# Optimization experiments

Hardware: AMD Instinct MI355X
Metric: run time of the kernel (lower is better)

## Reference

```python
import jax, jax.numpy as jnp
import numpy as np
from jax import lax

# Fixed dims from MSSMamba defaults
B_, L_, DM = 2, 8192, 256
NH, HP, NS = 4, 64, 8          # nheads, headdim, d_state
DIN = NH * HP                  # d_inner = 256
DPROJ = 2 * DIN + 2 * NS + NH  # 532


def setup_inputs() -> dict:
    key = jax.random.key(0)
    ks = jax.random.split(key, 16)
    f = lambda k, s, sc=1.0: jax.random.normal(k, s, jnp.float32) * sc
    inp = {
        'x_H': f(ks[0], (B_, L_, DM)),
        'x_V': f(ks[1], (B_, L_, DM)),
        'W_in_H': f(ks[2], (DM, 2 * DPROJ), 0.05),
        'W_in_V': f(ks[3], (DM, 2 * DPROJ), 0.05),
        'W_out_HF': f(ks[4], (DIN, DM), 0.05),
        'W_out_HB': f(ks[5], (DIN, DM), 0.05),
        'W_out_VF': f(ks[6], (DIN, DM), 0.05),
        'W_out_VB': f(ks[7], (DIN, DM), 0.05),
        'W_out': f(ks[8], (4 * DM, DM), 0.05),
    }
    for i, nm in enumerate(['HF', 'HB', 'VF', 'VB']):
        kd = jax.random.fold_in(ks[9], i)
        ka = jax.random.fold_in(ks[10], i)
        inp['dt_bias_' + nm] = f(kd, (NH,), 0.1)
        inp['A_log_' + nm] = jnp.log(jax.random.uniform(ka, (NH,), jnp.float32, 1.0, 16.0))
        inp['D_' + nm] = jnp.ones((NH,), jnp.float32)
    # per-batch permutation mapping vertical position -> horizontal position
    inp['v2h'] = jax.vmap(lambda k: jax.random.permutation(k, L_))(
        jax.random.split(ks[11], B_)).astype(jnp.int32)
    return inp


def _scan_dir(zxbcdt, dt_bias, A_log, D):
    # zxbcdt: [b, l, DPROJ] -> Mamba2-style selective scan, ngroups=1
    z = zxbcdt[..., :DIN].reshape(B_, L_, NH, HP)
    xBC = jax.nn.silu(zxbcdt[..., DIN:DIN + DIN + 2 * NS])
    x = xBC[..., :DIN].reshape(B_, L_, NH, HP)
    Bm = xBC[..., DIN:DIN + NS]      # [b, l, n]
    Cm = xBC[..., DIN + NS:]         # [b, l, n]
    dt = jax.nn.softplus(zxbcdt[..., -NH:] + dt_bias)  # [b, l, h]
    A = -jnp.exp(A_log)              # [h]
    dA = jnp.exp(dt * A)             # [b, l, h]
    dBx = jnp.einsum('blh,bln,blhp->blhpn', dt, Bm, x)  # [b,l,h,p,n]

    def step(state, inp):
        dA_t, dBx_t, C_t = inp
        state = dA_t[..., None, None] * state + dBx_t   # [b,h,p,n]
        y_t = jnp.einsum('bhpn,bn->bhp', state, C_t)
        return state, y_t

    init = jnp.zeros((B_, NH, HP, NS), dt.dtype)
    _, ys = lax.scan(step, init, (jnp.moveaxis(dA, 1, 0),
                                  jnp.moveaxis(dBx, 1, 0),
                                  jnp.moveaxis(Cm, 1, 0)))
    y = jnp.moveaxis(ys, 0, 1) + D[None, None, :, None] * x  # skip D*x
    y = y * jax.nn.silu(z)                                   # gate
    return y.reshape(B_, L_, DIN)


def reference(x_H, x_V, W_in_H, W_in_V,
              dt_bias_HF, dt_bias_HB, dt_bias_VF, dt_bias_VB,
              A_log_HF, A_log_HB, A_log_VF, A_log_VB,
              D_HF, D_HB, D_VF, D_VB,
              W_out_HF, W_out_HB, W_out_VF, W_out_VB,
              W_out, v2h):
    zx_HF, zx_HB = jnp.split(x_H @ W_in_H, 2, axis=-1)
    zx_VF, zx_VB = jnp.split(x_V @ W_in_V, 2, axis=-1)
    # note: source applies out_proj_HB to the HF branch (kept faithful)
    y_HF = _scan_dir(zx_HF, dt_bias_HF, A_log_HF, D_HF) @ W_out_HB
    y_HB = _scan_dir(zx_HB[:, ::-1], dt_bias_HB, A_log_HB, D_HB)[:, ::-1] @ W_out_HF
    y_VF = _scan_dir(zx_VF, dt_bias_VF, A_log_VF, D_VF) @ W_out_VB
    y_VB = _scan_dir(zx_VB[:, ::-1], dt_bias_VB, A_log_VB, D_VB)[:, ::-1] @ W_out_VF
    # remap vertical-ordered outputs to horizontal ordering (scatter by v2h)
    bidx = jnp.arange(B_)[:, None]
    y_VF = jnp.zeros_like(y_VF).at[bidx, v2h].set(y_VF)
    y_VB = jnp.zeros_like(y_VB).at[bidx, v2h].set(y_VB)
    cat = jnp.concatenate([y_HF, y_HB, y_VF, y_VB], axis=-1)  # [b, l, 4*d_model]
    return jax.nn.silu(cat) @ W_out
```

## Files before the change

### kernel.cpp

```cpp
#include <hip/hip_runtime.h>
#include <hip/hip_bf16.h>

#define B_N 2
#define L_N 8192
#define ROWS 16384
#define CHUNK 32
#define NCHUNK 256
#define NPAD 1152

typedef __bf16 bf16x8 __attribute__((ext_vector_type(8)));
typedef float f32x4 __attribute__((ext_vector_type(4)));

__device__ __forceinline__ float siluf(float v) {
  return v * __builtin_amdgcn_rcpf(1.f + __expf(-v));
}
__device__ __forceinline__ float softplusf_(float v) {
  return fmaxf(v, 0.f) + log1pf(__expf(-fabsf(v)));
}
__device__ __forceinline__ unsigned short f2bf(float v) {
  union { __bf16 b; unsigned short u; } x;
  x.b = (__bf16)v;
  return x.u;
}
__device__ __forceinline__ float bf2f(unsigned short u) {
  union { unsigned u; float f; } x; x.u = ((unsigned)u) << 16;
  return x.f;
}

__device__ __forceinline__ void gload_lds16(const unsigned short* g, unsigned short* l) {
  __builtin_amdgcn_global_load_lds(
      (const __attribute__((address_space(1))) unsigned int*)g,
      (__attribute__((address_space(3))) unsigned int*)l, 16, 0, 0);
}

struct P4 { const float* p[4]; };

__global__ void k_prep_all(const float* __restrict__ xH, const float* __restrict__ xV,
                           const float* __restrict__ WH, const float* __restrict__ WV,
                           P4 ws, const float* __restrict__ W_out, const int* __restrict__ v2h,
                           unsigned short* __restrict__ xbf, unsigned short* __restrict__ Wt_in,
                           unsigned short* __restrict__ Wt_dirs, unsigned short* __restrict__ Wt_fin,
                           int* __restrict__ inv) {
  int bid = blockIdx.x;
  int tid = threadIdx.x;
  if (bid < 8192) {
    int mat = bid >> 12;
    int i = (bid & 4095) * 256 + tid;
    const float* s = mat ? xV : xH;
    float4 v = ((const float4*)s)[i];
    ushort4 o;
    o.x = f2bf(v.x); o.y = f2bf(v.y); o.z = f2bf(v.z); o.w = f2bf(v.w);
    ((ushort4*)(xbf + (size_t)mat * ROWS * 256))[i] = o;
  } else if (bid < 10496) {
    int i = (bid - 8192) * 256 + tid;
    int z = i / (NPAD * 256);
    int rem = i - z * (NPAD * 256);
    int n = rem >> 8, k = rem & 255;
    const float* W = z ? WV : WH;
    int sl = n >= 544;
    int cc = n - (sl ? 544 : 0);
    float v = (cc < 532) ? W[(long)k * 1064 + sl * 532 + cc] : 0.f;
    Wt_in[i] = f2bf(v);
  } else if (bid < 11520) {
    int i = (bid - 10496) * 256 + tid;
    int d = i >> 16;
    int rem = i & 65535;
    int n = rem >> 8, k = rem & 255;
    Wt_dirs[i] = f2bf(ws.p[d][(long)k * 256 + n]);
  } else if (bid < 12544) {
    int i = (bid - 11520) * 256 + tid;
    int n = i >> 10, k = i & 1023;
    Wt_fin[i] = f2bf(W_out[(long)k * 256 + n]);
  } else {
    int m = (bid - 12544) * 256 + tid;
    if (m < ROWS) {
      int b = m >> 13;
      inv[b * L_N + v2h[m]] = m;
    }
  }
}

struct ScanConsts {
  const float* dt_bias[4];
  const float* A_log[4];
  const float* D[4];
};

__global__ __launch_bounds__(256) void k_dtfix(
    const float* __restrict__ xH, const float* __restrict__ xV,
    const float* __restrict__ WH, const float* __restrict__ WV,
    ScanConsts sc, float* __restrict__ dtv_arr, float* __restrict__ dA_arr) {
  __shared__ float xs[32][257];
  __shared__ float Wsm[8][260];
  const int mat = blockIdx.y;
  const float* x = mat ? xV : xH;
  const float* W = mat ? WV : WH;
  const int r0 = blockIdx.x * 32;
  for (int i = threadIdx.x; i < 2048; i += 256) {
    int c = i >> 8, k = i & 255;
    int sl = c >> 2, h = c & 3;
    Wsm[c][k] = W[(long)k * 1064 + sl * 532 + 528 + h];
  }
  for (int i = threadIdx.x; i < 32 * 64; i += 256) {
    int rl = i >> 6, kq = (i & 63) * 4;
    float4 v = *(const float4*)(x + (long)(r0 + rl) * 256 + kq);
    xs[rl][kq + 0] = v.x; xs[rl][kq + 1] = v.y; xs[rl][kq + 2] = v.z; xs[rl][kq + 3] = v.w;
  }
  __syncthreads();
  const int rl = threadIdx.x >> 3, c = threadIdx.x & 7;
  float s = 0.f;
  #pragma unroll 8
  for (int k = 0; k < 256; ++k) s = fmaf(xs[rl][k], Wsm[c][k], s);
  const int sl = c >> 2, h = c & 3;
  const int dir = mat * 2 + sl;
  float dtv = softplusf_(s + sc.dt_bias[dir][h]);
  float dAv = __expf(dtv * (-__expf(sc.A_log[dir][h])));
  long o = ((long)dir * 4 + h) * ROWS + (r0 + rl);
  dtv_arr[o] = dtv;
  dA_arr[o] = dAv;
}

struct EpiIn {
  unsigned short* zsil;
  unsigned short* xsil;
  unsigned short* bc;
};

__global__ __launch_bounds__(256) void k_gemm_in(
    const unsigned short* __restrict__ Abase, const unsigned short* __restrict__ Btbase,
    EpiIn ep) {
  __shared__ unsigned short As[128 * 32];
  __shared__ unsigned short Bs[128 * 32];
  __shared__ unsigned short trs[4][16 * 72];
  const int tid = threadIdx.x;
  const int lane = tid & 63;
  const int wid = tid >> 6;
  const int wm = wid & 1, wn = wid >> 1;
  const int q = lane >> 4, r = lane & 15;
  const int m0 = blockIdx.x * 128;
  const int n0 = blockIdx.y * 128;
  const int z = blockIdx.z;
  const unsigned short* A = Abase + (long)z * ROWS * 256;
  const unsigned short* Bt = Btbase + (long)z * NPAD * 256;

  f32x4 acc[4][4] = {};
  const int swr = (r >> 1) & 3;

  for (int kt = 0; kt < 256; kt += 32) {
    #pragma unroll
    for (int i = 0; i < 2; ++i) {
      int idx = i * 256 + tid;
      int row = idx >> 2;
      int ch = (idx & 3) ^ ((row >> 1) & 3);
      gload_lds16(A + (long)(m0 + row) * 256 + kt + ch * 8,
                  &As[(size_t)(i * 256 + wid * 64) * 8]);
    }
    #pragma unroll
    for (int i = 0; i < 2; ++i) {
      int idx = i * 256 + tid;
      int row = idx >> 2;
      int ch = (idx & 3) ^ ((row >> 1) & 3);
      gload_lds16(Bt + (long)(n0 + row) * 256 + kt + ch * 8,
                  &Bs[(size_t)(i * 256 + wid * 64) * 8]);
    }
    __syncthreads();
    bf16x8 af[4], bfr[4];
    #pragma unroll
    for (int mi = 0; mi < 4; ++mi)
      af[mi] = *(const bf16x8*)&As[((wm * 64 + mi * 16 + r) * 4 + (q ^ swr)) * 8];
    #pragma unroll
    for (int ni = 0; ni < 4; ++ni)
      bfr[ni] = *(const bf16x8*)&Bs[((wn * 64 + ni * 16 + r) * 4 + (q ^ swr)) * 8];
    #pragma unroll
    for (int mi = 0; mi < 4; ++mi)
      #pragma unroll
      for (int ni = 0; ni < 4; ++ni)
        acc[mi][ni] = __builtin_amdgcn_mfma_f32_16x16x32_bf16(af[mi], bfr[ni], acc[mi][ni], 0, 0, 0);
    __syncthreads();
  }

  unsigned short* tr = trs[wid];
  #pragma unroll
  for (int mi = 0; mi < 4; ++mi) {
    #pragma unroll
    for (int ni = 0; ni < 4; ++ni)
      #pragma unroll
      for (int j = 0; j < 4; ++j)
        tr[(q * 4 + j) * 72 + ni * 16 + r] = f2bf(siluf(acc[mi][ni][j]));
    asm volatile("s_waitcnt lgkmcnt(0)" ::: "memory");
    #pragma unroll
    for (int pass = 0; pass < 2; ++pass) {
      int rl = pass * 8 + (lane >> 3);
      int c8 = (lane & 7) * 8;
      bf16x8 v = *(const bf16x8*)&tr[rl * 72 + c8];
      int row = m0 + wm * 64 + mi * 16 + rl;
      int col = n0 + wn * 64 + c8;
      int sl = col >= 544;
      int cc = col - (sl ? 544 : 0);
      if (cc < 528) {
        int dir = z * 2 + sl;
        if (cc < 256)
          *(bf16x8*)(ep.zsil + ((long)dir * ROWS + row) * 256 + cc) = v;
        else if (cc < 512)
          *(bf16x8*)(ep.xsil + ((long)dir * ROWS + row) * 256 + cc - 256) = v;
        else
          *(bf16x8*)(ep.bc + ((long)dir * ROWS + row) * 16 + cc - 512) = v;
      }
    }
    asm volatile("s_waitcnt lgkmcnt(0)" ::: "memory");
  }
}

__global__ __launch_bounds__(256) void k_fuse(
    const unsigned short* __restrict__ ybf,
    const unsigned short* __restrict__ Wt_dirs,
    const unsigned short* __restrict__ Wt_fin,
    const int* __restrict__ inv,
    unsigned short* __restrict__ pbuf) {
  __shared__ unsigned short Tl[64][264];
  __shared__ unsigned short As1[64 * 32];
  __shared__ unsigned short Bs1[256 * 32];
  __shared__ int arow[64];
  const int tid = threadIdx.x;
  const int lane = tid & 63;
  const int wid = tid >> 6;
  const int q = lane >> 4, r = lane & 15;
  const int r0 = blockIdx.x * 64;
  const int pair = blockIdx.y;
  const int swr = (r >> 1) & 3;

  if (tid < 64) arow[tid] = pair ? inv[r0 + tid] : (r0 + tid);
  __syncthreads();

  f32x4 acc_o[4][4] = {};

  #pragma unroll
  for (int dd = 0; dd < 2; ++dd) {
    const int d = pair * 2 + dd;
    const unsigned short* yd = ybf + (long)d * ROWS * 256;
    const unsigned short* Wd = Wt_dirs + (long)d * 65536;

    f32x4 acc_t[4][4] = {};
    for (int kt = 0; kt < 256; kt += 32) {
      {
        int row = tid >> 2;
        int ch = (tid & 3) ^ ((row >> 1) & 3);
        gload_lds16(yd + (long)arow[row] * 256 + kt + ch * 8, &As1[(size_t)(wid * 64) * 8]);
      }
      #pragma unroll
      for (int i = 0; i < 4; ++i) {
        int idx = i * 256 + tid;
        int row = idx >> 2;
        int ch = (idx & 3) ^ ((row >> 1) & 3);
        gload_lds16(Wd + (long)row * 256 + kt + ch * 8,
                    &Bs1[(size_t)(i * 256 + wid * 64) * 8]);
      }
      __syncthreads();
      bf16x8 af[4], bfr[4];
      #pragma unroll
      for (int mi = 0; mi < 4; ++mi)
        af[mi] = *(const bf16x8*)&As1[((mi * 16 + r) * 4 + (q ^ swr)) * 8];
      #pragma unroll
      for (int ni = 0; ni < 4; ++ni)
        bfr[ni] = *(const bf16x8*)&Bs1[((wid * 64 + ni * 16 + r) * 4 + (q ^ swr)) * 8];
      #pragma unroll
      for (int mi = 0; mi < 4; ++mi)
        #pragma unroll
        for (int ni = 0; ni < 4; ++ni)
          acc_t[mi][ni] = __builtin_amdgcn_mfma_f32_16x16x32_bf16(af[mi], bfr[ni], acc_t[mi][ni], 0, 0, 0);
      __syncthreads();
    }
    #pragma unroll
    for (int mi = 0; mi < 4; ++mi)
      #pragma unroll
      for (int ni = 0; ni < 4; ++ni)
        #pragma unroll
        for (int j = 0; j < 4; ++j)
          Tl[mi * 16 + q * 4 + j][wid * 64 + ni * 16 + r] = f2bf(siluf(acc_t[mi][ni][j]));
    __syncthreads();
    for (int kt = 0; kt < 256; kt += 32) {
      #pragma unroll
      for (int i = 0; i < 4; ++i) {
        int idx = i * 256 + tid;
        int row = idx >> 2;
        int ch = (idx & 3) ^ ((row >> 1) & 3);
        gload_lds16(Wt_fin + (long)row * 1024 + d * 256 + kt + ch * 8,
                    &Bs1[(size_t)(i * 256 + wid * 64) * 8]);
      }
      __syncthreads();
      bf16x8 af[4], bfr[4];
      #pragma unroll
      for (int mi = 0; mi < 4; ++mi)
        af[mi] = *(const bf16x8*)&Tl[mi * 16 + r][kt + q * 8];
      #pragma unroll
      for (int ni = 0; ni < 4; ++ni)
        bfr[ni] = *(const bf16x8*)&Bs1[((wid * 64 + ni * 16 + r) * 4 + (q ^ swr)) * 8];
      #pragma unroll
      for (int mi = 0; mi < 4; ++mi)
        #pragma unroll
        for (int ni = 0; ni < 4; ++ni)
          acc_o[mi][ni] = __builtin_amdgcn_mfma_f32_16x16x32_bf16(af[mi], bfr[ni], acc_o[mi][ni], 0, 0, 0);
      __syncthreads();
    }
  }

  #pragma unroll
  for (int mi = 0; mi < 4; ++mi)
    #pragma unroll
    for (int ni = 0; ni < 4; ++ni)
      #pragma unroll
      for (int j = 0; j < 4; ++j)
        Tl[mi * 16 + q * 4 + j][wid * 64 + ni * 16 + r] = f2bf(acc_o[mi][ni][j]);
  asm volatile("s_waitcnt lgkmcnt(0)" ::: "memory");
  unsigned short* pout = pbuf + (long)pair * ROWS * 256;
  #pragma unroll
  for (int pass = 0; pass < 8; ++pass) {
    int rl = pass * 8 + (lane >> 3);
    int c8 = (lane & 7) * 8;
    bf16x8 v = *(const bf16x8*)&Tl[rl][wid * 64 + c8];
    *(bf16x8*)(pout + (long)(r0 + rl) * 256 + wid * 64 + c8) = v;
  }
}

__global__ void k_red(const unsigned short* __restrict__ pbuf, float* __restrict__ out) {
  int i = blockIdx.x * 256 + threadIdx.x;
  uint4 a = ((const uint4*)pbuf)[i];
  uint4 b = ((const uint4*)(pbuf + (size_t)ROWS * 256))[i];
  const unsigned short* au = (const unsigned short*)&a;
  const unsigned short* bu = (const unsigned short*)&b;
  float rr[8];
  #pragma unroll
  for (int j = 0; j < 8; ++j) rr[j] = bf2f(au[j]) + bf2f(bu[j]);
  ((float4*)out)[i * 2] = *(float4*)&rr[0];
  ((float4*)out)[i * 2 + 1] = *(float4*)&rr[4];
}

struct ScanP {
  const unsigned short* xsil;
  const unsigned short* zsil;
  const unsigned short* bc;
  const float* dtv;
  const float* dA;
  const float* D[4];
};

__global__ __launch_bounds__(64) void k_scan1(ScanP sp, float* __restrict__ S,
                                              float* __restrict__ P) {
  __shared__ __align__(16) float Bst[CHUNK][8];
  __shared__ float dAs[CHUNK];
  const int p = threadIdx.x;
  const int c = blockIdx.x;
  const int bh = blockIdx.y;
  const int d = blockIdx.z;
  const int b = bh >> 2, h = bh & 3;
  const int rev = d & 1;
  const int t0 = c * CHUNK;
  if (p < CHUNK) {
    const int t = t0 + p;
    const int l = rev ? (L_N - 1 - t) : t;
    const int row = (b << 13) + l;
    uint4 bv = *(const uint4*)(sp.bc + ((long)d * ROWS + row) * 16);
    const unsigned short* bu = (const unsigned short*)&bv;
    float dtvv = sp.dtv[((long)d * 4 + h) * ROWS + row];
    dAs[p] = sp.dA[((long)d * 4 + h) * ROWS + row];
    #pragma unroll
    for (int n = 0; n < 8; ++n) Bst[p][n] = bf2f(bu[n]) * dtvv;
  }
  __syncthreads();

  float st[8] = {0, 0, 0, 0, 0, 0, 0, 0};
  float cumdA = 1.f;
  const int l0 = rev ? (L_N - 1 - t0) : t0;
  const unsigned short* xp = sp.xsil + ((long)d * ROWS + (b << 13) + l0) * 256 + h * 64 + p;
  const long stp = rev ? -256L : 256L;

  unsigned short xa[8], xb[8];
  #pragma unroll
  for (int j = 0; j < 8; ++j) xa[j] = xp[(long)j * stp];
  #pragma unroll
  for (int g = 0; g < 4; ++g) {
    if (g < 3) {
      #pragma unroll
      for (int j = 0; j < 8; ++j) xb[j] = xp[(long)((g + 1) * 8 + j) * stp];
    }
    #pragma unroll
    for (int j = 0; j < 8; ++j) {
      int s = g * 8 + j;
      float x = bf2f(xa[j]);
      float dA = dAs[s];
      f32x4 B0 = *(const f32x4*)&Bst[s][0];
      f32x4 B1 = *(const f32x4*)&Bst[s][4];
      cumdA *= dA;
      st[0] = fmaf(dA, st[0], x * B0[0]);
      st[1] = fmaf(dA, st[1], x * B0[1]);
      st[2] = fmaf(dA, st[2], x * B0[2]);
      st[3] = fmaf(dA, st[3], x * B0[3]);
      st[4] = fmaf(dA, st[4], x * B1[0]);
      st[5] = fmaf(dA, st[5], x * B1[1]);
      st[6] = fmaf(dA, st[6], x * B1[2]);
      st[7] = fmaf(dA, st[7], x * B1[3]);
    }
    #pragma unroll
    for (int j = 0; j < 8; ++j) xa[j] = xb[j];
  }
  float* Sp = S + ((((long)d * NCHUNK + c) * 8 + bh) * 64 + p) * 8;
  #pragma unroll
  for (int n = 0; n < 8; ++n) Sp[n] = st[n];
  if (p == 0) P[((long)d * NCHUNK + c) * 8 + bh] = cumdA;
}

__global__ __launch_bounds__(512) void k_scan2(const float* __restrict__ S,
                                               const float* __restrict__ P,
                                               float* __restrict__ carry) {
  __shared__ float Pl[NCHUNK];
  const int tid = threadIdx.x;
  const int dbh = blockIdx.x;
  const int d = dbh >> 3, bh = dbh & 7;
  if (tid < NCHUNK) Pl[tid] = P[((long)d * NCHUNK + tid) * 8 + bh];
  __syncthreads();
  float cy = 0.f;
  carry[(((long)d * NCHUNK + 0) * 8 + bh) * 512 + tid] = 0.f;
  #pragma unroll 8
  for (int c = 1; c < NCHUNK; ++c) {
    const float Sv = S[(((long)d * NCHUNK + (c - 1)) * 8 + bh) * 512 + tid];
    cy = fmaf(Pl[c - 1], cy, Sv);
    carry[(((long)d * NCHUNK + c) * 8 + bh) * 512 + tid] = cy;
  }
}

__global__ __launch_bounds__(64) void k_scan3(ScanP sp, const float* __restrict__ carry,
                                              unsigned short* __restrict__ ybf) {
  __shared__ __align__(16) float Bst[CHUNK][8];
  __shared__ __align__(16) float Cst[CHUNK][8];
  __shared__ float dAs[CHUNK];
  const int p = threadIdx.x;
  const int c = blockIdx.x;
  const int bh = blockIdx.y;
  const int d = blockIdx.z;
  const int b = bh >> 2, h = bh & 3;
  const int rev = d & 1;
  const float Dv = sp.D[d][h];
  const int t0 = c * CHUNK;
  if (p < CHUNK) {
    const int t = t0 + p;
    const int l = rev ? (L_N - 1 - t) : t;
    const int row = (b << 13) + l;
    const unsigned short* bp = sp.bc + ((long)d * ROWS + row) * 16;
    uint4 bv = *(const uint4*)bp;
    uint4 cv = *(const uint4*)(bp + 8);
    const unsigned short* bu = (const unsigned short*)&bv;
    const unsigned short* cu = (const unsigned short*)&cv;
    float dtvv = sp.dtv[((long)d * 4 + h) * ROWS + row];
    dAs[p] = sp.dA[((long)d * 4 + h) * ROWS + row];
    #pragma unroll
    for (int n = 0; n < 8; ++n) Bst[p][n] = bf2f(bu[n]) * dtvv;
    #pragma unroll
    for (int n = 0; n < 8; ++n) Cst[p][n] = bf2f(cu[n]);
  }
  __syncthreads();

  float st[8];
  {
    const float* cp = carry + ((((long)d * NCHUNK + c) * 8 + bh) * 64 + p) * 8;
    #pragma unroll
    for (int n = 0; n < 8; ++n) st[n] = cp[n];
  }

  const int l0 = rev ? (L_N - 1 - t0) : t0;
  const long base = (long)(b << 13) + l0;
  const unsigned short* xp = sp.xsil + ((long)d * ROWS + base) * 256 + h * 64 + p;
  const unsigned short* zp = sp.zsil + ((long)d * ROWS + base) * 256 + h * 64 + p;
  unsigned short* yp = ybf + ((long)d * ROWS + base) * 256 + h * 64 + p;
  const long stp = rev ? -256L : 256L;

  unsigned short xa[8], xb[8], za[8], zb[8];
  #pragma unroll
  for (int j = 0; j < 8; ++j) { xa[j] = xp[(long)j * stp]; za[j] = zp[(long)j * stp]; }
  #pragma unroll
  for (int g = 0; g < 4; ++g) {
    if (g < 3) {
      #pragma unroll
      for (int j = 0; j < 8; ++j) {
        xb[j] = xp[(long)((g + 1) * 8 + j) * stp];
        zb[j] = zp[(long)((g + 1) * 8 + j) * stp];
      }
    }
    #pragma unroll
    for (int j = 0; j < 8; ++j) {
      int s = g * 8 + j;
      float x = bf2f(xa[j]);
      float zv = bf2f(za[j]);
      float dA = dAs[s];
      f32x4 B0 = *(const f32x4*)&Bst[s][0];
      f32x4 B1 = *(const f32x4*)&Bst[s][4];
      f32x4 C0 = *(const f32x4*)&Cst[s][0];
      f32x4 C1 = *(const f32x4*)&Cst[s][4];
      st[0] = fmaf(dA, st[0], x * B0[0]);
      st[1] = fmaf(dA, st[1], x * B0[1]);
      st[2] = fmaf(dA, st[2], x * B0[2]);
      st[3] = fmaf(dA, st[3], x * B0[3]);
      st[4] = fmaf(dA, st[4], x * B1[0]);
      st[5] = fmaf(dA, st[5], x * B1[1]);
      st[6] = fmaf(dA, st[6], x * B1[2]);
      st[7] = fmaf(dA, st[7], x * B1[3]);
      float y01 = fmaf(st[1], C0[1], st[0] * C0[0]);
      float y23 = fmaf(st[3], C0[3], st[2] * C0[2]);
      float y45 = fmaf(st[5], C1[1], st[4] * C1[0]);
      float y67 = fmaf(st[7], C1[3], st[6] * C1[2]);
      float y = (y01 + y23) + (y45 + y67);
      y = fmaf(Dv, x, y) * zv;
      yp[(long)s * stp] = f2bf(y);
    }
    #pragma unroll
    for (int j = 0; j < 8; ++j) { xa[j] = xb[j]; za[j] = zb[j]; }
  }
}

extern "C" void kernel_launch(void* const* d_in, const int* in_sizes, int n_in,
                              void* d_out, int out_size, void* d_ws, size_t ws_size,
                              hipStream_t stream) {
  const float* x_H = (const float*)d_in[0];
  const float* x_V = (const float*)d_in[1];
  const float* W_in_H = (const float*)d_in[2];
  const float* W_in_V = (const float*)d_in[3];
  const float* W_out_HF = (const float*)d_in[4];
  const float* W_out_HB = (const float*)d_in[5];
  const float* W_out_VF = (const float*)d_in[6];
  const float* W_out_VB = (const float*)d_in[7];
  const float* W_out = (const float*)d_in[8];
  const float* dt_bias_HF = (const float*)d_in[9];
  const float* A_log_HF = (const float*)d_in[10];
  const float* D_HF = (const float*)d_in[11];
  const float* dt_bias_HB = (const float*)d_in[12];
  const float* A_log_HB = (const float*)d_in[13];
  const float* D_HB = (const float*)d_in[14];
  const float* dt_bias_VF = (const float*)d_in[15];
  const float* A_log_VF = (const float*)d_in[16];
  const float* D_VF = (const float*)d_in[17];
  const float* dt_bias_VB = (const float*)d_in[18];
  const float* A_log_VB = (const float*)d_in[19];
  const float* D_VB = (const float*)d_in[20];
  const int* v2h = (const int*)d_in[21];

  char* ws = (char*)d_ws;
  size_t off = 0;
  auto alloc = [&](size_t bytes) {
    void* pp = ws + off;
    off = (off + bytes + 255) & ~(size_t)255;
    return pp;
  };
  unsigned short* xbf = (unsigned short*)alloc((size_t)2 * ROWS * 256 * 2);
  unsigned short* Wt_in = (unsigned short*)alloc((size_t)2 * NPAD * 256 * 2);
  unsigned short* Wt_dirs = (unsigned short*)alloc((size_t)4 * 65536 * 2);
  unsigned short* Wt_fin = (unsigned short*)alloc((size_t)256 * 1024 * 2);
  unsigned short* zsil = (unsigned short*)alloc((size_t)4 * ROWS * 256 * 2);
  unsigned short* xsil = (unsigned short*)alloc((size_t)4 * ROWS * 256 * 2);
  unsigned short* bc = (unsigned short*)alloc((size_t)4 * ROWS * 16 * 2);
  float* dtv_arr = (float*)alloc((size_t)16 * ROWS * 4);
  float* dA_arr = (float*)alloc((size_t)16 * ROWS * 4);
  unsigned short* ybf = (unsigned short*)alloc((size_t)4 * ROWS * 256 * 2);
  float* S = (float*)alloc((size_t)4 * NCHUNK * 8 * 512 * 4);
  float* P = (float*)alloc((size_t)4 * NCHUNK * 8 * 4);
  float* carry = (float*)alloc((size_t)4 * NCHUNK * 8 * 512 * 4);
  int* inv = (int*)alloc((size_t)ROWS * 4);
  unsigned short* pbuf = (unsigned short*)alloc((size_t)2 * ROWS * 256 * 2);

  P4 wdirs;
  wdirs.p[0] = W_out_HB; wdirs.p[1] = W_out_HF; wdirs.p[2] = W_out_VB; wdirs.p[3] = W_out_VF;
  k_prep_all<<<12608, 256, 0, stream>>>(x_H, x_V, W_in_H, W_in_V, wdirs, W_out, v2h,
                                        xbf, Wt_in, Wt_dirs, Wt_fin, inv);

  ScanConsts sc;
  sc.dt_bias[0] = dt_bias_HF; sc.dt_bias[1] = dt_bias_HB;
  sc.dt_bias[2] = dt_bias_VF; sc.dt_bias[3] = dt_bias_VB;
  sc.A_log[0] = A_log_HF; sc.A_log[1] = A_log_HB;
  sc.A_log[2] = A_log_VF; sc.A_log[3] = A_log_VB;
  sc.D[0] = D_HF; sc.D[1] = D_HB; sc.D[2] = D_VF; sc.D[3] = D_VB;

  EpiIn ep; ep.zsil = zsil; ep.xsil = xsil; ep.bc = bc;

  k_gemm_in<<<dim3(ROWS / 128, NPAD / 128, 2), 256, 0, stream>>>(xbf, Wt_in, ep);
  k_dtfix<<<dim3(ROWS / 32, 2), 256, 0, stream>>>(x_H, x_V, W_in_H, W_in_V, sc, dtv_arr, dA_arr);

  ScanP sp;
  sp.xsil = xsil; sp.zsil = zsil; sp.bc = bc; sp.dtv = dtv_arr; sp.dA = dA_arr;
  sp.D[0] = D_HF; sp.D[1] = D_HB; sp.D[2] = D_VF; sp.D[3] = D_VB;

  k_scan1<<<dim3(NCHUNK, 8, 4), 64, 0, stream>>>(sp, S, P);
  k_scan2<<<32, 512, 0, stream>>>(S, P, carry);
  k_scan3<<<dim3(NCHUNK, 8, 4), 64, 0, stream>>>(sp, carry, ybf);

  k_fuse<<<dim3(ROWS / 64, 2), 256, 0, stream>>>(ybf, Wt_dirs, Wt_fin, inv, pbuf);
  k_red<<<ROWS * 256 / 8 / 256, 256, 0, stream>>>(pbuf, (float*)d_out);

  (void)in_sizes; (void)n_in; (void)out_size; (void)ws_size;
}
```

Measured before the change: 271.2 us.

## Fuse x bf16 conversion into dtfix and defer SiLU from GEMM epilogue to scans

The fp32-to-bf16 conversion of x_H/x_V moves out of k_prep_all and into k_dtfix, which already loads those rows into shared memory, so x is read from global memory once instead of twice. k_dtfix now runs before the input GEMM so xbf is ready in time. The input GEMM epilogue stores raw pre-activation values, and SiLU is applied inside the scan kernels on load. This removes activation work from the GEMM epilogue, but x's SiLU is now computed twice (once in scan1 and once in scan3), and rounding to bf16 happens before SiLU instead of after.

Measured after the change: 273.0 us. About the same (+0.7%).

```diff
diff --git a/kernel.cpp b/kernel.cpp
--- a/kernel.cpp
+++ b/kernel.cpp
@@ -35,24 +35,15 @@
 
 struct P4 { const float* p[4]; };
 
-__global__ void k_prep_all(const float* __restrict__ xH, const float* __restrict__ xV,
-                           const float* __restrict__ WH, const float* __restrict__ WV,
+__global__ void k_prep_all(const float* __restrict__ WH, const float* __restrict__ WV,
                            P4 ws, const float* __restrict__ W_out, const int* __restrict__ v2h,
-                           unsigned short* __restrict__ xbf, unsigned short* __restrict__ Wt_in,
+                           unsigned short* __restrict__ Wt_in,
                            unsigned short* __restrict__ Wt_dirs, unsigned short* __restrict__ Wt_fin,
                            int* __restrict__ inv) {
   int bid = blockIdx.x;
   int tid = threadIdx.x;
-  if (bid < 8192) {
-    int mat = bid >> 12;
-    int i = (bid & 4095) * 256 + tid;
-    const float* s = mat ? xV : xH;
-    float4 v = ((const float4*)s)[i];
-    ushort4 o;
-    o.x = f2bf(v.x); o.y = f2bf(v.y); o.z = f2bf(v.z); o.w = f2bf(v.w);
-    ((ushort4*)(xbf + (size_t)mat * ROWS * 256))[i] = o;
-  } else if (bid < 10496) {
-    int i = (bid - 8192) * 256 + tid;
+  if (bid < 2304) {
+    int i = bid * 256 + tid;
     int z = i / (NPAD * 256);
     int rem = i - z * (NPAD * 256);
     int n = rem >> 8, k = rem & 255;
@@ -61,18 +52,18 @@
     int cc = n - (sl ? 544 : 0);
     float v = (cc < 532) ? W[(long)k * 1064 + sl * 532 + cc] : 0.f;
     Wt_in[i] = f2bf(v);
-  } else if (bid < 11520) {
-    int i = (bid - 10496) * 256 + tid;
+  } else if (bid < 3328) {
+    int i = (bid - 2304) * 256 + tid;
     int d = i >> 16;
     int rem = i & 65535;
     int n = rem >> 8, k = rem & 255;
     Wt_dirs[i] = f2bf(ws.p[d][(long)k * 256 + n]);
-  } else if (bid < 12544) {
-    int i = (bid - 11520) * 256 + tid;
+  } else if (bid < 4352) {
+    int i = (bid - 3328) * 256 + tid;
     int n = i >> 10, k = i & 1023;
     Wt_fin[i] = f2bf(W_out[(long)k * 256 + n]);
   } else {
-    int m = (bid - 12544) * 256 + tid;
+    int m = (bid - 4352) * 256 + tid;
     if (m < ROWS) {
       int b = m >> 13;
       inv[b * L_N + v2h[m]] = m;
@@ -89,7 +80,8 @@
 __global__ __launch_bounds__(256) void k_dtfix(
     const float* __restrict__ xH, const float* __restrict__ xV,
     const float* __restrict__ WH, const float* __restrict__ WV,
-    ScanConsts sc, float* __restrict__ dtv_arr, float* __restrict__ dA_arr) {
+    ScanConsts sc, float* __restrict__ dtv_arr, float* __restrict__ dA_arr,
+    unsigned short* __restrict__ xbf) {
   __shared__ float xs[32][257];
   __shared__ float Wsm[8][260];
   const int mat = blockIdx.y;
@@ -107,6 +99,15 @@
     xs[rl][kq + 0] = v.x; xs[rl][kq + 1] = v.y; xs[rl][kq + 2] = v.z; xs[rl][kq + 3] = v.w;
   }
   __syncthreads();
+  for (int i = threadIdx.x; i < 32 * 64; i += 256) {
+    int rl = i >> 6, kq = (i & 63) * 4;
+    ushort4 o;
+    o.x = f2bf(xs[rl][kq + 0]);
+    o.y = f2bf(xs[rl][kq + 1]);
+    o.z = f2bf(xs[rl][kq + 2]);
+    o.w = f2bf(xs[rl][kq + 3]);
+    *(ushort4*)(xbf + (size_t)mat * ROWS * 256 + (long)(r0 + rl) * 256 + kq) = o;
+  }
   const int rl = threadIdx.x >> 3, c = threadIdx.x & 7;
   float s = 0.f;
   #pragma unroll 8
@@ -121,8 +122,8 @@
 }
 
 struct EpiIn {
-  unsigned short* zsil;
-  unsigned short* xsil;
+  unsigned short* zraw;
+  unsigned short* xraw;
   unsigned short* bc;
 };
 
@@ -186,7 +187,7 @@
     for (int ni = 0; ni < 4; ++ni)
       #pragma unroll
       for (int j = 0; j < 4; ++j)
-        tr[(q * 4 + j) * 72 + ni * 16 + r] = f2bf(siluf(acc[mi][ni][j]));
+        tr[(q * 4 + j) * 72 + ni * 16 + r] = f2bf(acc[mi][ni][j]);
     asm volatile("s_waitcnt lgkmcnt(0)" ::: "memory");
     #pragma unroll
     for (int pass = 0; pass < 2; ++pass) {
@@ -200,9 +201,9 @@
       if (cc < 528) {
         int dir = z * 2 + sl;
         if (cc < 256)
-          *(bf16x8*)(ep.zsil + ((long)dir * ROWS + row) * 256 + cc) = v;
+          *(bf16x8*)(ep.zraw + ((long)dir * ROWS + row) * 256 + cc) = v;
         else if (cc < 512)
-          *(bf16x8*)(ep.xsil + ((long)dir * ROWS + row) * 256 + cc - 256) = v;
+          *(bf16x8*)(ep.xraw + ((long)dir * ROWS + row) * 256 + cc - 256) = v;
         else
           *(bf16x8*)(ep.bc + ((long)dir * ROWS + row) * 16 + cc - 512) = v;
       }
@@ -336,8 +337,8 @@
 }
 
 struct ScanP {
-  const unsigned short* xsil;
-  const unsigned short* zsil;
+  const unsigned short* xraw;
+  const unsigned short* zraw;
   const unsigned short* bc;
   const float* dtv;
   const float* dA;
@@ -364,14 +365,14 @@
     float dtvv = sp.dtv[((long)d * 4 + h) * ROWS + row];
     dAs[p] = sp.dA[((long)d * 4 + h) * ROWS + row];
     #pragma unroll
-    for (int n = 0; n < 8; ++n) Bst[p][n] = bf2f(bu[n]) * dtvv;
+    for (int n = 0; n < 8; ++n) Bst[p][n] = siluf(bf2f(bu[n])) * dtvv;
   }
   __syncthreads();
 
   float st[8] = {0, 0, 0, 0, 0, 0, 0, 0};
   float cumdA = 1.f;
   const int l0 = rev ? (L_N - 1 - t0) : t0;
-  const unsigned short* xp = sp.xsil + ((long)d * ROWS + (b << 13) + l0) * 256 + h * 64 + p;
+  const unsigned short* xp = sp.xraw + ((long)d * ROWS + (b << 13) + l0) * 256 + h * 64 + p;
   const long stp = rev ? -256L : 256L;
 
   unsigned short xa[8], xb[8];
@@ -386,7 +387,7 @@
     #pragma unroll
     for (int j = 0; j < 8; ++j) {
       int s = g * 8 + j;
-      float x = bf2f(xa[j]);
+      float x = siluf(bf2f(xa[j]));
       float dA = dAs[s];
       f32x4 B0 = *(const f32x4*)&Bst[s][0];
       f32x4 B1 = *(const f32x4*)&Bst[s][4];
@@ -453,9 +454,9 @@
     float dtvv = sp.dtv[((long)d * 4 + h) * ROWS + row];
     dAs[p] = sp.dA[((long)d * 4 + h) * ROWS + row];
     #pragma unroll
-    for (int n = 0; n < 8; ++n) Bst[p][n] = bf2f(bu[n]) * dtvv;
-    #pragma unroll
-    for (int n = 0; n < 8; ++n) Cst[p][n] = bf2f(cu[n]);
+    for (int n = 0; n < 8; ++n) Bst[p][n] = siluf(bf2f(bu[n])) * dtvv;
+    #pragma unroll
+    for (int n = 0; n < 8; ++n) Cst[p][n] = siluf(bf2f(cu[n]));
   }
   __syncthreads();
 
@@ -468,8 +469,8 @@
 
   const int l0 = rev ? (L_N - 1 - t0) : t0;
   const long base = (long)(b << 13) + l0;
-  const unsigned short* xp = sp.xsil + ((long)d * ROWS + base) * 256 + h * 64 + p;
-  const unsigned short* zp = sp.zsil + ((long)d * ROWS + base) * 256 + h * 64 + p;
+  const unsigned short* xp = sp.xraw + ((long)d * ROWS + base) * 256 + h * 64 + p;
+  const unsigned short* zp = sp.zraw + ((long)d * ROWS + base) * 256 + h * 64 + p;
   unsigned short* yp = ybf + ((long)d * ROWS + base) * 256 + h * 64 + p;
   const long stp = rev ? -256L : 256L;
 
@@ -488,8 +489,8 @@
     #pragma unroll
     for (int j = 0; j < 8; ++j) {
       int s = g * 8 + j;
-      float x = bf2f(xa[j]);
-      float zv = bf2f(za[j]);
+      float x = siluf(bf2f(xa[j]));
+      float zv = siluf(bf2f(za[j]));
       float dA = dAs[s];
       f32x4 B0 = *(const f32x4*)&Bst[s][0];
       f32x4 B1 = *(const f32x4*)&Bst[s][4];
@@ -553,8 +554,8 @@
   unsigned short* Wt_in = (unsigned short*)alloc((size_t)2 * NPAD * 256 * 2);
   unsigned short* Wt_dirs = (unsigned short*)alloc((size_t)4 * 65536 * 2);
   unsigned short* Wt_fin = (unsigned short*)alloc((size_t)256 * 1024 * 2);
-  unsigned short* zsil = (unsigned short*)alloc((size_t)4 * ROWS * 256 * 2);
-  unsigned short* xsil = (unsigned short*)alloc((size_t)4 * ROWS * 256 * 2);
+  unsigned short* zraw = (unsigned short*)alloc((size_t)4 * ROWS * 256 * 2);
+  unsigned short* xraw = (unsigned short*)alloc((size_t)4 * ROWS * 256 * 2);
   unsigned short* bc = (unsigned short*)alloc((size_t)4 * ROWS * 16 * 2);
   float* dtv_arr = (float*)alloc((size_t)16 * ROWS * 4);
   float* dA_arr = (float*)alloc((size_t)16 * ROWS * 4);
@@ -565,11 +566,6 @@
   int* inv = (int*)alloc((size_t)ROWS * 4);
   unsigned short* pbuf = (unsigned short*)alloc((size_t)2 * ROWS * 256 * 2);
 
-  P4 wdirs;
-  wdirs.p[0] = W_out_HB; wdirs.p[1] = W_out_HF; wdirs.p[2] = W_out_VB; wdirs.p[3] = W_out_VF;
-  k_prep_all<<<12608, 256, 0, stream>>>(x_H, x_V, W_in_H, W_in_V, wdirs, W_out, v2h,
-                                        xbf, Wt_in, Wt_dirs, Wt_fin, inv);
-
   ScanConsts sc;
   sc.dt_bias[0] = dt_bias_HF; sc.dt_bias[1] = dt_bias_HB;
   sc.dt_bias[2] = dt_bias_VF; sc.dt_bias[3] = dt_bias_VB;
@@ -577,13 +573,19 @@
   sc.A_log[2] = A_log_VF; sc.A_log[3] = A_log_VB;
   sc.D[0] = D_HF; sc.D[1] = D_HB; sc.D[2] = D_VF; sc.D[3] = D_VB;
 
-  EpiIn ep; ep.zsil = zsil; ep.xsil = xsil; ep.bc = bc;
+  P4 wdirs;
+  wdirs.p[0] = W_out_HB; wdirs.p[1] = W_out_HF; wdirs.p[2] = W_out_VB; wdirs.p[3] = W_out_VF;
+  k_prep_all<<<4416, 256, 0, stream>>>(W_in_H, W_in_V, wdirs, W_out, v2h,
+                                       Wt_in, Wt_dirs, Wt_fin, inv);
+  k_dtfix<<<dim3(ROWS / 32, 2), 256, 0, stream>>>(x_H, x_V, W_in_H, W_in_V, sc,
+                                                  dtv_arr, dA_arr, xbf);
+
+  EpiIn ep; ep.zraw = zraw; ep.xraw = xraw; ep.bc = bc;
 
   k_gemm_in<<<dim3(ROWS / 128, NPAD / 128, 2), 256, 0, stream>>>(xbf, Wt_in, ep);
-  k_dtfix<<<dim3(ROWS / 32, 2), 256, 0, stream>>>(x_H, x_V, W_in_H, W_in_V, sc, dtv_arr, dA_arr);
 
   ScanP sp;
-  sp.xsil = xsil; sp.zsil = zsil; sp.bc = bc; sp.dtv = dtv_arr; sp.dA = dA_arr;
+  sp.xraw = xraw; sp.zraw = zraw; sp.bc = bc; sp.dtv = dtv_arr; sp.dA = dA_arr;
   sp.D[0] = D_HF; sp.D[1] = D_HB; sp.D[2] = D_VF; sp.D[3] = D_VB;
 
   k_scan1<<<dim3(NCHUNK, 8, 4), 64, 0, stream>>>(sp, S, P);
```
